# Kernel optimization log

Measured on AMD Instinct MI355X. Metric: run time of the kernel, lower is better.

The kernel has to match this reference:

```python
import jax, jax.numpy as jnp
import numpy as np

EPS = 1e-5
NUM_GROUPS = 32
NUM_HEADS = 4


def setup_inputs() -> dict:
    key = jax.random.key(0)
    ks = jax.random.split(key, 3)
    B, C, H, W = 4, 256, 64, 64
    x = jax.random.normal(ks[0], (B, C, H, W), dtype=jnp.float32)
    gn_w = jnp.ones((C,), jnp.float32)
    gn_b = jnp.zeros((C,), jnp.float32)
    qkv_w = jax.random.normal(ks[1], (3 * C, C), dtype=jnp.float32) * (C ** -0.5)
    qkv_b = jnp.zeros((3 * C,), jnp.float32)
    proj_w = jax.random.normal(ks[2], (C, C), dtype=jnp.float32) * (C ** -0.5)
    proj_b = jnp.zeros((C,), jnp.float32)
    return {"x": x, "gn_w": gn_w, "gn_b": gn_b, "qkv_w": qkv_w,
            "qkv_b": qkv_b, "proj_w": proj_w, "proj_b": proj_b}


def _group_norm(x, w, b):
    B, C, H, W = x.shape
    xg = x.reshape(B, NUM_GROUPS, C // NUM_GROUPS, H, W)
    mean = xg.mean(axis=(2, 3, 4), keepdims=True)
    var = xg.var(axis=(2, 3, 4), keepdims=True)
    xn = ((xg - mean) * jax.lax.rsqrt(var + EPS)).reshape(B, C, H, W)
    return xn * w[None, :, None, None] + b[None, :, None, None]


def reference(x, gn_w, gn_b, qkv_w, qkv_b, proj_w, proj_b):
    B, C, H, W = x.shape
    nh = NUM_HEADS
    d = C // nh
    L = H * W
    h = _group_norm(x, gn_w, gn_b)
    # 1x1 conv == channel matmul
    qkv = jnp.einsum('oc,bchw->bohw', qkv_w, h) + qkv_b[None, :, None, None]
    q, k, v = jnp.split(qkv, 3, axis=1)
    # (B, C, H, W) -> (B, nh, L, d)
    def to_heads(t):
        return t.reshape(B, nh, d, L).transpose(0, 1, 3, 2)
    q, k, v = to_heads(q), to_heads(k), to_heads(v)
    scale = d ** -0.5
    attn = jax.nn.softmax(jnp.einsum('bhqd,bhkd->bhqk', q, k) * scale, axis=-1)
    o = jnp.einsum('bhqk,bhkd->bhqd', attn, v)          # (B, nh, L, d)
    o = o.transpose(0, 1, 3, 2).reshape(B, C, H, W)
    o = jnp.einsum('oc,bchw->bohw', proj_w, o) + proj_b[None, :, None, None]
    return x + o
```

## Files before the change

kernel.cpp:

```cpp
#include <hip/hip_runtime.h>

#define B_   4
#define C_   256
#define L_   4096
#define NH_  4
#define D_   64
#define G_   32
#define CPG_ 8

typedef __bf16 bf16x8 __attribute__((ext_vector_type(8)));
typedef float  f32x4  __attribute__((ext_vector_type(4)));

__device__ __forceinline__ ushort f2bf(float f) {
  union { float f; unsigned u; } c; c.f = f;
  unsigned u = c.u;
  return (ushort)((u + 0x7fffu + ((u >> 16) & 1u)) >> 16);
}
__device__ __forceinline__ float bf2f(ushort h) {
  union { unsigned u; float f; } c; c.u = ((unsigned)h) << 16; return c.f;
}
__device__ __forceinline__ unsigned fbits(float f) {
  union { float f; unsigned u; } c; c.f = f; return c.u;
}
__device__ __forceinline__ float fastexp2(float x) {
#if __has_builtin(__builtin_amdgcn_exp2f)
  return __builtin_amdgcn_exp2f(x);
#else
  return exp2f(x);
#endif
}

__global__ __launch_bounds__(256) void pre_kernel(const float* __restrict__ x,
                                                  const float* __restrict__ wqf,
                                                  const float* __restrict__ wpf,
                                                  ushort* __restrict__ wq,
                                                  ushort* __restrict__ wp,
                                                  float* __restrict__ stats2) {
  int bidx = blockIdx.x;
  int tid  = threadIdx.x;
  if (bidx >= 1024) {
    int t = (bidx - 1024) * 256 + tid;
    const int NQ4 = (768 * 256) / 4;
    float4 v;
    if (t < NQ4) {
      v = ((const float4*)wqf)[t];
      ((ushort4*)wq)[t] = make_ushort4(f2bf(v.x), f2bf(v.y), f2bf(v.z), f2bf(v.w));
    } else {
      int i = t - NQ4;
      v = ((const float4*)wpf)[i];
      ((ushort4*)wp)[i] = make_ushort4(f2bf(v.x), f2bf(v.y), f2bf(v.z), f2bf(v.w));
    }
    return;
  }
  int bg = bidx >> 3, chunk = bidx & 7;
  int b = bg >> 5, g = bg & 31;
  const float* xg = x + ((size_t)b * C_ + g * CPG_) * L_ + chunk * 512;

  float s = 0.f, ss = 0.f;
  for (int c = 0; c < CPG_; ++c) {
    float2 v = ((const float2*)(xg + (size_t)c * L_))[tid];
    s  += v.x + v.y;
    ss += v.x * v.x + v.y * v.y;
  }
  for (int off = 32; off; off >>= 1) { s += __shfl_xor(s, off); ss += __shfl_xor(ss, off); }
  __shared__ float red[8];
  int w = tid >> 6;
  if ((tid & 63) == 0) { red[w] = s; red[4 + w] = ss; }
  __syncthreads();
  if (tid == 0) {
    stats2[bidx * 2]     = red[0] + red[1] + red[2] + red[3];
    stats2[bidx * 2 + 1] = red[4] + red[5] + red[6] + red[7];
  }
}

__global__ __launch_bounds__(256) void qkv_kernel(const float* __restrict__ x,
                                                  const float* __restrict__ stats2,
                                                  const float* __restrict__ gw,
                                                  const float* __restrict__ gb,
                                                  const ushort* __restrict__ w,
                                                  const float* __restrict__ bias,
                                                  ushort* __restrict__ q,
                                                  ushort* __restrict__ k,
                                                  ushort* __restrict__ v) {
  __shared__ __align__(16) ushort h_lds[32][264];

  int tid  = threadIdx.x;
  int wv_  = tid >> 6, lane = tid & 63;
  int quad = lane >> 4, col = lane & 15;
  int bid  = (int)blockIdx.x;
  int b    = bid >> 7;
  int lt   = bid & 127;
  int l0   = lt * 32;

  {
    int ll = tid & 31, chunk = tid >> 5;
    int c0 = chunk * 32;
    const float inv_n = 1.0f / (CPG_ * L_);
    float mean[4], rstd[4];
#pragma unroll
    for (int gg = 0; gg < 4; ++gg) {
      int bg = b * 32 + chunk * 4 + gg;
      float s = 0.f, ss = 0.f;
#pragma unroll
      for (int c2 = 0; c2 < 8; ++c2) {
        s  += stats2[(bg * 8 + c2) * 2];
        ss += stats2[(bg * 8 + c2) * 2 + 1];
      }
      mean[gg] = s * inv_n;
      float var = ss * inv_n - mean[gg] * mean[gg];
      rstd[gg] = rsqrtf(var + 1e-5f);
    }
    int l = l0 + ll;
    union { uint4 u[4]; ushort s[32]; } o;
#pragma unroll
    for (int c = 0; c < 32; ++c) {
      int gg = c >> 3;
      float wvv = gw[c0 + c], bvv = gb[c0 + c];
      float val = x[((size_t)b * C_ + c0 + c) * L_ + l];
      o.s[c] = f2bf((val - mean[gg]) * rstd[gg] * wvv + bvv);
    }
#pragma unroll
    for (int i = 0; i < 4; ++i)
      *(uint4*)&h_lds[ll][c0 + i * 8] = o.u[i];
  }
  __syncthreads();

#pragma unroll
  for (int p = 0; p < 3; ++p) {
    int ot = wv_ + 4 * p;
    int o0 = ot * 64;
    const ushort* abase = w + (size_t)(o0 + col) * C_ + quad * 8;

    f32x4 acc[4][2];
    for (int i = 0; i < 4; ++i) for (int j = 0; j < 2; ++j)
      acc[i][j] = (f32x4){0.f, 0.f, 0.f, 0.f};

#pragma unroll
    for (int k0 = 0; k0 < C_; k0 += 32) {
      bf16x8 a[4], bb[2];
#pragma unroll
      for (int i = 0; i < 4; ++i) a[i]  = *(const bf16x8*)(abase + (size_t)(i * 16) * C_ + k0);
#pragma unroll
      for (int j = 0; j < 2; ++j) bb[j] = *(const bf16x8*)&h_lds[j * 16 + col][k0 + quad * 8];
#pragma unroll
      for (int i = 0; i < 4; ++i)
#pragma unroll
        for (int j = 0; j < 2; ++j)
          acc[i][j] = __builtin_amdgcn_mfma_f32_16x16x32_bf16(a[i], bb[j], acc[i][j], 0, 0, 0);
    }

    int third = o0 >> 8;
    int hh    = (o0 & 255) >> 6;
    float scale = (third == 0) ? 0.180336880111120f : 1.0f;
#pragma unroll
    for (int i = 0; i < 4; ++i) {
      int oo = o0 + i * 16 + quad * 4;
      int dd = i * 16 + quad * 4;
#pragma unroll
      for (int j = 0; j < 2; ++j) {
        int l = l0 + j * 16 + col;
        ushort pk[4];
        for (int r = 0; r < 4; ++r) pk[r] = f2bf((acc[i][j][r] + bias[oo + r]) * scale);
        if (third < 2) {
          ushort* dst = (third ? k : q) + (((size_t)(b * NH_ + hh) * L_ + l) * D_ + dd);
          *(ushort4*)dst = make_ushort4(pk[0], pk[1], pk[2], pk[3]);
        } else {
          for (int r = 0; r < 4; ++r)
            v[((size_t)(b * NH_ + hh) * D_ + dd + r) * L_ + l] = pk[r];
        }
      }
    }
  }
}

__global__ __launch_bounds__(256, 2) void attn_kernel(const ushort* __restrict__ q,
                                                      const ushort* __restrict__ k,
                                                      const ushort* __restrict__ v,
                                                      ushort* __restrict__ p0,
                                                      ushort* __restrict__ p1,
                                                      float* __restrict__ psumbuf) {
  __shared__ __align__(16) ushort k_lds[2][64][72];
  __shared__ __align__(16) ushort v_lds[2][64][72];

  int tid   = threadIdx.x;
  int w     = tid >> 6, lane = tid & 63;
  int quad  = lane >> 4, col = lane & 15;
  int bid   = (int)blockIdx.x;
  bid = (bid & 7) * 64 + (bid >> 3);
  int split = bid >> 8;
  int bh    = (bid >> 4) & 15;
  int qblk  = bid & 15;

  const ushort* qp = q + (size_t)bh * L_ * D_;
  const ushort* kp = k + (size_t)bh * L_ * D_;
  const ushort* vp = v + (size_t)bh * D_ * L_;

  int qrow0 = qblk * 256 + w * 64;
  bf16x8 bq[4][2];
#pragma unroll
  for (int f = 0; f < 4; ++f)
#pragma unroll
    for (int c = 0; c < 2; ++c)
      bq[f][c] = *(const bf16x8*)(qp + (size_t)(qrow0 + f * 16 + col) * D_ + c * 32 + quad * 8);

  f32x4 oacc[4][4];
#pragma unroll
  for (int f = 0; f < 4; ++f)
    for (int t = 0; t < 4; ++t) oacc[f][t] = (f32x4){0.f, 0.f, 0.f, 0.f};
  f32x4 pacc[4];
#pragma unroll
  for (int f = 0; f < 4; ++f) pacc[f] = (f32x4){0.f, 0.f, 0.f, 0.f};
  const f32x4 Z = (f32x4){0.f, 0.f, 0.f, 0.f};

  union { ushort s[8]; bf16x8 v8; } one_u;
#pragma unroll
  for (int i = 0; i < 8; ++i) one_u.s[i] = 0x3F80;
  bf16x8 ones = one_u.v8;

  int vrow = tid >> 2, vchunk = tid & 3;
  int vwoff = (vchunk >> 1) * 32 + (vchunk & 1) * 4;
  int kt0 = split * (L_ / 2), kt_end = kt0 + L_ / 2;

  {
    const uint4* ksrc = (const uint4*)(kp + (size_t)kt0 * D_);
    uint4 a  = ksrc[tid];
    uint4 b2 = ksrc[tid + 256];
    const uint4* vsrc = (const uint4*)(vp + (size_t)vrow * L_ + kt0);
    uint4 c0 = vsrc[vchunk * 2];
    uint4 c1 = vsrc[vchunk * 2 + 1];
    *(uint4*)&k_lds[0][tid >> 3][(tid & 7) * 8] = a;
    *(uint4*)&k_lds[0][32 + (tid >> 3)][(tid & 7) * 8] = b2;
    ushort* vb = &v_lds[0][vrow][vwoff];
    *(uint2*)(vb + 0)  = make_uint2(c0.x, c0.y);
    *(uint2*)(vb + 8)  = make_uint2(c0.z, c0.w);
    *(uint2*)(vb + 16) = make_uint2(c1.x, c1.y);
    *(uint2*)(vb + 24) = make_uint2(c1.z, c1.w);
  }
  __syncthreads();

  int cur = 0;
  for (int kt = kt0; kt < kt_end; kt += 64) {
    bool has_next = (kt + 64) < kt_end;

    f32x4 s[2][4][2];
    __builtin_amdgcn_s_setprio(1);
#pragma unroll
    for (int h = 0; h < 2; ++h) {
      bf16x8 a00 = *(const bf16x8*)&k_lds[cur][h * 32 + col][quad * 8];
      bf16x8 a01 = *(const bf16x8*)&k_lds[cur][h * 32 + col][32 + quad * 8];
      bf16x8 a10 = *(const bf16x8*)&k_lds[cur][h * 32 + 16 + col][quad * 8];
      bf16x8 a11 = *(const bf16x8*)&k_lds[cur][h * 32 + 16 + col][32 + quad * 8];
#pragma unroll
      for (int f = 0; f < 4; ++f) {
        s[h][f][0] = __builtin_amdgcn_mfma_f32_16x16x32_bf16(a00, bq[f][0], Z, 0, 0, 0);
        s[h][f][1] = __builtin_amdgcn_mfma_f32_16x16x32_bf16(a10, bq[f][0], Z, 0, 0, 0);
        s[h][f][0] = __builtin_amdgcn_mfma_f32_16x16x32_bf16(a01, bq[f][1], s[h][f][0], 0, 0, 0);
        s[h][f][1] = __builtin_amdgcn_mfma_f32_16x16x32_bf16(a11, bq[f][1], s[h][f][1], 0, 0, 0);
      }
    }
    __builtin_amdgcn_s_setprio(0);

    uint4 nk0, nk1, nv0, nv1;
    if (has_next) {
      const uint4* ksrc = (const uint4*)(kp + (size_t)(kt + 64) * D_);
      nk0 = ksrc[tid];
      nk1 = ksrc[tid + 256];
      const uint4* vsrc = (const uint4*)(vp + (size_t)vrow * L_ + (kt + 64));
      nv0 = vsrc[vchunk * 2];
      nv1 = vsrc[vchunk * 2 + 1];
    }

#pragma unroll
    for (int h = 0; h < 2; ++h) {
      bf16x8 pb[4];
#pragma unroll
      for (int f = 0; f < 4; ++f) {
        float pe0[4], pe1[4];
#pragma unroll
        for (int r = 0; r < 4; ++r) {
          pe0[r] = fastexp2(s[h][f][0][r]);
          pe1[r] = fastexp2(s[h][f][1][r]);
        }
        union { unsigned u[4]; bf16x8 v8; } pc;
        pc.u[0] = __builtin_amdgcn_perm(fbits(pe0[1]), fbits(pe0[0]), 0x07060302u);
        pc.u[1] = __builtin_amdgcn_perm(fbits(pe0[3]), fbits(pe0[2]), 0x07060302u);
        pc.u[2] = __builtin_amdgcn_perm(fbits(pe1[1]), fbits(pe1[0]), 0x07060302u);
        pc.u[3] = __builtin_amdgcn_perm(fbits(pe1[3]), fbits(pe1[2]), 0x07060302u);
        pb[f] = pc.v8;
      }
#pragma unroll
      for (int f = 0; f < 4; ++f)
        pacc[f] = __builtin_amdgcn_mfma_f32_16x16x32_bf16(ones, pb[f], pacc[f], 0, 0, 0);
#pragma unroll
      for (int t = 0; t < 4; ++t) {
        bf16x8 av = *(const bf16x8*)&v_lds[cur][t * 16 + col][h * 32 + quad * 8];
#pragma unroll
        for (int f = 0; f < 4; ++f)
          oacc[f][t] = __builtin_amdgcn_mfma_f32_16x16x32_bf16(av, pb[f], oacc[f][t], 0, 0, 0);
      }
    }

    if (has_next) {
      int nb = cur ^ 1;
      *(uint4*)&k_lds[nb][tid >> 3][(tid & 7) * 8] = nk0;
      *(uint4*)&k_lds[nb][32 + (tid >> 3)][(tid & 7) * 8] = nk1;
      ushort* vb = &v_lds[nb][vrow][vwoff];
      *(uint2*)(vb + 0)  = make_uint2(nv0.x, nv0.y);
      *(uint2*)(vb + 8)  = make_uint2(nv0.z, nv0.w);
      *(uint2*)(vb + 16) = make_uint2(nv1.x, nv1.y);
      *(uint2*)(vb + 24) = make_uint2(nv1.z, nv1.w);
      __syncthreads();
      cur = nb;
    }
  }

  ushort* po = split ? p1 : p0;
#pragma unroll
  for (int f = 0; f < 4; ++f) {
    for (int t = 0; t < 4; ++t) {
      ushort ok[4];
      for (int r = 0; r < 4; ++r) ok[r] = f2bf(oacc[f][t][r]);
      ushort* dst = po + ((size_t)bh * L_ + qrow0 + f * 16 + col) * D_ + t * 16 + quad * 4;
      *(ushort4*)dst = make_ushort4(ok[0], ok[1], ok[2], ok[3]);
    }
    if (quad == 0)
      psumbuf[split * (16 * L_) + bh * L_ + qrow0 + f * 16 + col] = pacc[f][0];
  }
}

__global__ __launch_bounds__(256) void comb_kernel(ushort* __restrict__ p0,
                                                   const ushort* __restrict__ p1,
                                                   const float* __restrict__ ps) {
  int idx = blockIdx.x * 256 + threadIdx.x;
  int row = idx >> 3;
  float inv = 1.0f / (ps[row] + ps[16 * L_ + row]);
  union { uint4 u; ushort s[8]; } ua, ub, o;
  ua.u = ((const uint4*)p0)[idx];
  ub.u = ((const uint4*)p1)[idx];
#pragma unroll
  for (int e = 0; e < 8; ++e)
    o.s[e] = f2bf((bf2f(ua.s[e]) + bf2f(ub.s[e])) * inv);
  ((uint4*)p0)[idx] = o.u;
}

template<bool FUSED>
__global__ __launch_bounds__(256) void proj_kernel(const ushort* __restrict__ p0,
                                                   const ushort* __restrict__ p1,
                                                   const float* __restrict__ ps,
                                                   const ushort* __restrict__ pw,
                                                   const float* __restrict__ pb,
                                                   const float* __restrict__ x,
                                                   float* __restrict__ out) {
  __shared__ __align__(16) ushort a_lds[32][264];

  int tid  = threadIdx.x;
  int w    = tid >> 6, lane = tid & 63;
  int quad = lane >> 4, col = lane & 15;
  int bid  = (int)blockIdx.x;
  int oct  = (bid & 1) * 4 + w;
  int lt   = (bid >> 1) & 127;
  int b    = bid >> 8;
  int l0 = lt * 32, oc0 = oct * 32;

  if (FUSED) {
    int ll = tid & 31, chunk = tid >> 5;
    int hh = chunk >> 1, d0 = (chunk & 1) * 32;
    size_t row = (size_t)(b * NH_ + hh) * L_ + l0 + ll;
    float inv = 1.0f / (ps[row] + ps[16 * L_ + row]);
    const uint4* s0 = (const uint4*)(p0 + row * D_ + d0);
    const uint4* s1 = (const uint4*)(p1 + row * D_ + d0);
    union { uint4 u[4]; ushort s[32]; } ua, ub, o;
#pragma unroll
    for (int i = 0; i < 4; ++i) { ua.u[i] = s0[i]; ub.u[i] = s1[i]; }
#pragma unroll
    for (int e = 0; e < 32; ++e)
      o.s[e] = f2bf((bf2f(ua.s[e]) + bf2f(ub.s[e])) * inv);
#pragma unroll
    for (int i = 0; i < 4; ++i)
      *(uint4*)&a_lds[ll][chunk * 32 + i * 8] = o.u[i];
    __syncthreads();
  }

  f32x4 acc[2][2];
  for (int i = 0; i < 2; ++i) for (int j = 0; j < 2; ++j)
    acc[i][j] = (f32x4){0.f, 0.f, 0.f, 0.f};

#pragma unroll
  for (int k0 = 0; k0 < C_; k0 += 32) {
    int hh = k0 >> 6, dk = k0 & 63;
    bf16x8 a[2], bb[2];
#pragma unroll
    for (int i = 0; i < 2; ++i) {
      if (FUSED) {
        a[i] = *(const bf16x8*)&a_lds[i * 16 + col][k0 + quad * 8];
      } else {
        a[i] = *(const bf16x8*)(p0 + ((size_t)(b * NH_ + hh) * L_ + l0 + i * 16 + col) * D_ + dk + quad * 8);
      }
    }
#pragma unroll
    for (int j = 0; j < 2; ++j)
      bb[j] = *(const bf16x8*)(pw + (size_t)(oc0 + j * 16 + col) * C_ + k0 + quad * 8);
#pragma unroll
    for (int i = 0; i < 2; ++i)
#pragma unroll
      for (int j = 0; j < 2; ++j)
        acc[i][j] = __builtin_amdgcn_mfma_f32_16x16x32_bf16(a[i], bb[j], acc[i][j], 0, 0, 0);
  }

#pragma unroll
  for (int j = 0; j < 2; ++j) {
    int oc = oc0 + j * 16 + col;
    float bias = pb[oc];
#pragma unroll
    for (int i = 0; i < 2; ++i) {
      int l = l0 + i * 16 + quad * 4;
      size_t off = ((size_t)b * C_ + oc) * L_ + l;
      float4 xv = *(const float4*)(x + off);
      float4 ov = make_float4(acc[i][j][0] + bias + xv.x,
                              acc[i][j][1] + bias + xv.y,
                              acc[i][j][2] + bias + xv.z,
                              acc[i][j][3] + bias + xv.w);
      *(float4*)(out + off) = ov;
    }
  }
}

extern "C" void kernel_launch(void* const* d_in, const int* in_sizes, int n_in,
                              void* d_out, int out_size, void* d_ws, size_t ws_size,
                              hipStream_t stream) {
  const float* x      = (const float*)d_in[0];
  const float* gn_w   = (const float*)d_in[1];
  const float* gn_b   = (const float*)d_in[2];
  const float* qkv_w  = (const float*)d_in[3];
  const float* qkv_b  = (const float*)d_in[4];
  const float* proj_w = (const float*)d_in[5];
  const float* proj_b = (const float*)d_in[6];
  float* out = (float*)d_out;

  const size_t TEN = (size_t)B_ * C_ * L_;
  ushort* ws  = (ushort*)d_ws;
  ushort* q   = ws;
  ushort* k   = ws + TEN;
  ushort* v   = ws + 2 * TEN;
  ushort* oat = ws + 3 * TEN;
  ushort* wq  = ws + 4 * TEN;
  ushort* wp  = wq + 768 * 256;
  ushort* wend = wp + 256 * 256;
  float*  st2 = (float*)((ushort*)d_out + TEN);

  const size_t base_bytes  = (size_t)(wend - ws) * 2;
  const size_t need_fused  = base_bytes + TEN * 2  + (size_t)2 * 16 * L_ * 4 ;
  const bool   fused       = ws_size >= need_fused;

  pre_kernel <<<1280,      256, 0, stream>>>(x, qkv_w, proj_w, wq, wp, st2);
  qkv_kernel <<<512,       256, 0, stream>>>(x, st2, gn_w, gn_b, wq, qkv_b, q, k, v);

  if (fused) {
    ushort* p1w = wend;
    float*  psw = (float*)(wend + TEN);
    attn_kernel<<<512, 256, 0, stream>>>(q, k, v, oat, p1w, psw);
    proj_kernel<true><<<1024, 256, 0, stream>>>(oat, p1w, psw, wp, proj_b, x, out);
  } else {
    ushort* p1d = (ushort*)d_out + TEN;
    float*  psb = (float*)d_out;
    attn_kernel<<<512, 256, 0, stream>>>(q, k, v, oat, p1d, psb);
    comb_kernel<<<2048, 256, 0, stream>>>(oat, p1d, psb);
    proj_kernel<false><<<1024, 256, 0, stream>>>(oat, oat, psb, wp, proj_b, x, out);
  }
}
```

Measured before the change: 191.5 us.

## Merge all stages into one cooperative persistent kernel with grid syncs

Replaces the four separate launches (weight conversion and GroupNorm stats, QKV projection, split-K attention, output projection) with a single cooperative kernel of 512 blocks. Stages are separated by grid.sync(). This removes per-launch overhead and the gaps between kernels. In exchange, every stage now runs at a fixed grid of 512 blocks with two blocks per CU. Each grid barrier also costs time, and the later stages must loop over virtual blocks. If the cooperative launch fails, the code falls back to the old multi-kernel path.

```diff
diff --git a/kernel.cpp b/kernel.cpp
--- a/kernel.cpp
+++ b/kernel.cpp
@@ -1,4 +1,7 @@
 #include <hip/hip_runtime.h>
+#include <hip/hip_cooperative_groups.h>
+
+namespace cg = cooperative_groups;
 
 #define B_   4
 #define C_   256
@@ -28,6 +31,376 @@
 #else
   return exp2f(x);
 #endif
+}
+
+__global__ __launch_bounds__(256, 2) void mega_kernel(
+    const float* __restrict__ x,
+    const float* __restrict__ wqf, const float* __restrict__ wpf,
+    const float* __restrict__ gnw, const float* __restrict__ gnb,
+    const float* __restrict__ qbias, const float* __restrict__ pbias,
+    ushort* wq, ushort* wp, float* st2,
+    ushort* q, ushort* k, ushort* v,
+    ushort* oat, ushort* p1, float* ps,
+    float* out) {
+  __shared__ __align__(16) ushort sm_u[18432];
+
+  cg::grid_group grid = cg::this_grid();
+  int bid0 = (int)blockIdx.x;
+  int tid  = threadIdx.x;
+
+  {
+    float* red = (float*)sm_u;
+    for (int vb = bid0; vb < 1280; vb += 512) {
+      if (vb >= 1024) {
+        int t = (vb - 1024) * 256 + tid;
+        const int NQ4 = (768 * 256) / 4;
+        float4 vv;
+        if (t < NQ4) {
+          vv = ((const float4*)wqf)[t];
+          ((ushort4*)wq)[t] = make_ushort4(f2bf(vv.x), f2bf(vv.y), f2bf(vv.z), f2bf(vv.w));
+        } else {
+          int i = t - NQ4;
+          vv = ((const float4*)wpf)[i];
+          ((ushort4*)wp)[i] = make_ushort4(f2bf(vv.x), f2bf(vv.y), f2bf(vv.z), f2bf(vv.w));
+        }
+        continue;
+      }
+      int bg = vb >> 3, chunk = vb & 7;
+      int b = bg >> 5, g = bg & 31;
+      const float* xg = x + ((size_t)b * C_ + g * CPG_) * L_ + chunk * 512;
+      float s = 0.f, ss = 0.f;
+      for (int c = 0; c < CPG_; ++c) {
+        float2 vv = ((const float2*)(xg + (size_t)c * L_))[tid];
+        s  += vv.x + vv.y;
+        ss += vv.x * vv.x + vv.y * vv.y;
+      }
+      for (int off = 32; off; off >>= 1) { s += __shfl_xor(s, off); ss += __shfl_xor(ss, off); }
+      int w = tid >> 6;
+      if ((tid & 63) == 0) { red[w] = s; red[4 + w] = ss; }
+      __syncthreads();
+      if (tid == 0) {
+        st2[vb * 2]     = red[0] + red[1] + red[2] + red[3];
+        st2[vb * 2 + 1] = red[4] + red[5] + red[6] + red[7];
+      }
+      __syncthreads();
+    }
+  }
+  grid.sync();
+
+  {
+    typedef ushort HRow[264];
+    HRow* h_lds = (HRow*)sm_u;
+
+    int wv_  = tid >> 6, lane = tid & 63;
+    int quad = lane >> 4, col = lane & 15;
+    int b    = bid0 >> 7;
+    int lt   = bid0 & 127;
+    int l0   = lt * 32;
+
+    {
+      int ll = tid & 31, chunk = tid >> 5;
+      int c0 = chunk * 32;
+      const float inv_n = 1.0f / (CPG_ * L_);
+      float mean[4], rstd[4];
+#pragma unroll
+      for (int gg = 0; gg < 4; ++gg) {
+        int bg = b * 32 + chunk * 4 + gg;
+        float s = 0.f, ss = 0.f;
+#pragma unroll
+        for (int c2 = 0; c2 < 8; ++c2) {
+          s  += st2[(bg * 8 + c2) * 2];
+          ss += st2[(bg * 8 + c2) * 2 + 1];
+        }
+        mean[gg] = s * inv_n;
+        float var = ss * inv_n - mean[gg] * mean[gg];
+        rstd[gg] = rsqrtf(var + 1e-5f);
+      }
+      int l = l0 + ll;
+      union { uint4 u[4]; ushort s[32]; } o;
+#pragma unroll
+      for (int c = 0; c < 32; ++c) {
+        int gg = c >> 3;
+        float wvv = gnw[c0 + c], bvv = gnb[c0 + c];
+        float val = x[((size_t)b * C_ + c0 + c) * L_ + l];
+        o.s[c] = f2bf((val - mean[gg]) * rstd[gg] * wvv + bvv);
+      }
+#pragma unroll
+      for (int i = 0; i < 4; ++i)
+        *(uint4*)&h_lds[ll][c0 + i * 8] = o.u[i];
+    }
+    __syncthreads();
+
+#pragma unroll
+    for (int p = 0; p < 3; ++p) {
+      int ot = wv_ + 4 * p;
+      int o0 = ot * 64;
+      const ushort* abase = wq + (size_t)(o0 + col) * C_ + quad * 8;
+
+      f32x4 acc[4][2];
+      for (int i = 0; i < 4; ++i) for (int j = 0; j < 2; ++j)
+        acc[i][j] = (f32x4){0.f, 0.f, 0.f, 0.f};
+
+#pragma unroll
+      for (int k0 = 0; k0 < C_; k0 += 32) {
+        bf16x8 a[4], bb[2];
+#pragma unroll
+        for (int i = 0; i < 4; ++i) a[i]  = *(const bf16x8*)(abase + (size_t)(i * 16) * C_ + k0);
+#pragma unroll
+        for (int j = 0; j < 2; ++j) bb[j] = *(const bf16x8*)&h_lds[j * 16 + col][k0 + quad * 8];
+#pragma unroll
+        for (int i = 0; i < 4; ++i)
+#pragma unroll
+          for (int j = 0; j < 2; ++j)
+            acc[i][j] = __builtin_amdgcn_mfma_f32_16x16x32_bf16(a[i], bb[j], acc[i][j], 0, 0, 0);
+      }
+
+      int third = o0 >> 8;
+      int hh    = (o0 & 255) >> 6;
+      float scale = (third == 0) ? 0.180336880111120f : 1.0f;
+#pragma unroll
+      for (int i = 0; i < 4; ++i) {
+        int oo = o0 + i * 16 + quad * 4;
+        int dd = i * 16 + quad * 4;
+#pragma unroll
+        for (int j = 0; j < 2; ++j) {
+          int l = l0 + j * 16 + col;
+          ushort pk[4];
+          for (int r = 0; r < 4; ++r) pk[r] = f2bf((acc[i][j][r] + qbias[oo + r]) * scale);
+          if (third < 2) {
+            ushort* dst = (third ? k : q) + (((size_t)(b * NH_ + hh) * L_ + l) * D_ + dd);
+            *(ushort4*)dst = make_ushort4(pk[0], pk[1], pk[2], pk[3]);
+          } else {
+            for (int r = 0; r < 4; ++r)
+              v[((size_t)(b * NH_ + hh) * D_ + dd + r) * L_ + l] = pk[r];
+          }
+        }
+      }
+    }
+  }
+  grid.sync();
+
+  {
+    typedef ushort KArr[64][72];
+    KArr* k_lds = (KArr*)sm_u;
+    KArr* v_lds = (KArr*)(sm_u + 2 * 64 * 72);
+
+    int w     = tid >> 6, lane = tid & 63;
+    int quad  = lane >> 4, col = lane & 15;
+    int bid   = (bid0 & 7) * 64 + (bid0 >> 3);
+    int split = bid >> 8;
+    int bh    = (bid >> 4) & 15;
+    int qblk  = bid & 15;
+
+    const ushort* qp = q + (size_t)bh * L_ * D_;
+    const ushort* kp = k + (size_t)bh * L_ * D_;
+    const ushort* vp = v + (size_t)bh * D_ * L_;
+
+    int qrow0 = qblk * 256 + w * 64;
+    bf16x8 bq[4][2];
+#pragma unroll
+    for (int f = 0; f < 4; ++f)
+#pragma unroll
+      for (int c = 0; c < 2; ++c)
+        bq[f][c] = *(const bf16x8*)(qp + (size_t)(qrow0 + f * 16 + col) * D_ + c * 32 + quad * 8);
+
+    f32x4 oacc[4][4];
+#pragma unroll
+    for (int f = 0; f < 4; ++f)
+      for (int t = 0; t < 4; ++t) oacc[f][t] = (f32x4){0.f, 0.f, 0.f, 0.f};
+    f32x4 pacc[4];
+#pragma unroll
+    for (int f = 0; f < 4; ++f) pacc[f] = (f32x4){0.f, 0.f, 0.f, 0.f};
+    const f32x4 Z = (f32x4){0.f, 0.f, 0.f, 0.f};
+
+    union { ushort s[8]; bf16x8 v8; } one_u;
+#pragma unroll
+    for (int i = 0; i < 8; ++i) one_u.s[i] = 0x3F80;
+    bf16x8 ones = one_u.v8;
+
+    int vrow = tid >> 2, vchunk = tid & 3;
+    int vwoff = (vchunk >> 1) * 32 + (vchunk & 1) * 4;
+    int kt0 = split * (L_ / 2), kt_end = kt0 + L_ / 2;
+
+    {
+      const uint4* ksrc = (const uint4*)(kp + (size_t)kt0 * D_);
+      uint4 a  = ksrc[tid];
+      uint4 b2 = ksrc[tid + 256];
+      const uint4* vsrc = (const uint4*)(vp + (size_t)vrow * L_ + kt0);
+      uint4 c0 = vsrc[vchunk * 2];
+      uint4 c1 = vsrc[vchunk * 2 + 1];
+      *(uint4*)&k_lds[0][tid >> 3][(tid & 7) * 8] = a;
+      *(uint4*)&k_lds[0][32 + (tid >> 3)][(tid & 7) * 8] = b2;
+      ushort* vb = &v_lds[0][vrow][vwoff];
+      *(uint2*)(vb + 0)  = make_uint2(c0.x, c0.y);
+      *(uint2*)(vb + 8)  = make_uint2(c0.z, c0.w);
+      *(uint2*)(vb + 16) = make_uint2(c1.x, c1.y);
+      *(uint2*)(vb + 24) = make_uint2(c1.z, c1.w);
+    }
+    __syncthreads();
+
+    int cur = 0;
+    for (int kt = kt0; kt < kt_end; kt += 64) {
+      bool has_next = (kt + 64) < kt_end;
+
+      f32x4 s[2][4][2];
+      __builtin_amdgcn_s_setprio(1);
+#pragma unroll
+      for (int h = 0; h < 2; ++h) {
+        bf16x8 a00 = *(const bf16x8*)&k_lds[cur][h * 32 + col][quad * 8];
+        bf16x8 a01 = *(const bf16x8*)&k_lds[cur][h * 32 + col][32 + quad * 8];
+        bf16x8 a10 = *(const bf16x8*)&k_lds[cur][h * 32 + 16 + col][quad * 8];
+        bf16x8 a11 = *(const bf16x8*)&k_lds[cur][h * 32 + 16 + col][32 + quad * 8];
+#pragma unroll
+        for (int f = 0; f < 4; ++f) {
+          s[h][f][0] = __builtin_amdgcn_mfma_f32_16x16x32_bf16(a00, bq[f][0], Z, 0, 0, 0);
+          s[h][f][1] = __builtin_amdgcn_mfma_f32_16x16x32_bf16(a10, bq[f][0], Z, 0, 0, 0);
+          s[h][f][0] = __builtin_amdgcn_mfma_f32_16x16x32_bf16(a01, bq[f][1], s[h][f][0], 0, 0, 0);
+          s[h][f][1] = __builtin_amdgcn_mfma_f32_16x16x32_bf16(a11, bq[f][1], s[h][f][1], 0, 0, 0);
+        }
+      }
+      __builtin_amdgcn_s_setprio(0);
+
+      uint4 nk0, nk1, nv0, nv1;
+      if (has_next) {
+        const uint4* ksrc = (const uint4*)(kp + (size_t)(kt + 64) * D_);
+        nk0 = ksrc[tid];
+        nk1 = ksrc[tid + 256];
+        const uint4* vsrc = (const uint4*)(vp + (size_t)vrow * L_ + (kt + 64));
+        nv0 = vsrc[vchunk * 2];
+        nv1 = vsrc[vchunk * 2 + 1];
+      }
+
+#pragma unroll
+      for (int h = 0; h < 2; ++h) {
+        bf16x8 pb[4];
+#pragma unroll
+        for (int f = 0; f < 4; ++f) {
+          float pe0[4], pe1[4];
+#pragma unroll
+          for (int r = 0; r < 4; ++r) {
+            pe0[r] = fastexp2(s[h][f][0][r]);
+            pe1[r] = fastexp2(s[h][f][1][r]);
+          }
+          union { unsigned u[4]; bf16x8 v8; } pc;
+          pc.u[0] = __builtin_amdgcn_perm(fbits(pe0[1]), fbits(pe0[0]), 0x07060302u);
+          pc.u[1] = __builtin_amdgcn_perm(fbits(pe0[3]), fbits(pe0[2]), 0x07060302u);
+          pc.u[2] = __builtin_amdgcn_perm(fbits(pe1[1]), fbits(pe1[0]), 0x07060302u);
+          pc.u[3] = __builtin_amdgcn_perm(fbits(pe1[3]), fbits(pe1[2]), 0x07060302u);
+          pb[f] = pc.v8;
+        }
+#pragma unroll
+        for (int f = 0; f < 4; ++f)
+          pacc[f] = __builtin_amdgcn_mfma_f32_16x16x32_bf16(ones, pb[f], pacc[f], 0, 0, 0);
+#pragma unroll
+        for (int t = 0; t < 4; ++t) {
+          bf16x8 av = *(const bf16x8*)&v_lds[cur][t * 16 + col][h * 32 + quad * 8];
+#pragma unroll
+          for (int f = 0; f < 4; ++f)
+            oacc[f][t] = __builtin_amdgcn_mfma_f32_16x16x32_bf16(av, pb[f], oacc[f][t], 0, 0, 0);
+        }
+      }
+
+      if (has_next) {
+        int nb = cur ^ 1;
+        *(uint4*)&k_lds[nb][tid >> 3][(tid & 7) * 8] = nk0;
+        *(uint4*)&k_lds[nb][32 + (tid >> 3)][(tid & 7) * 8] = nk1;
+        ushort* vb = &v_lds[nb][vrow][vwoff];
+        *(uint2*)(vb + 0)  = make_uint2(nv0.x, nv0.y);
+        *(uint2*)(vb + 8)  = make_uint2(nv0.z, nv0.w);
+        *(uint2*)(vb + 16) = make_uint2(nv1.x, nv1.y);
+        *(uint2*)(vb + 24) = make_uint2(nv1.z, nv1.w);
+        __syncthreads();
+        cur = nb;
+      }
+    }
+
+    ushort* po = split ? p1 : oat;
+#pragma unroll
+    for (int f = 0; f < 4; ++f) {
+      for (int t = 0; t < 4; ++t) {
+        ushort ok[4];
+        for (int r = 0; r < 4; ++r) ok[r] = f2bf(oacc[f][t][r]);
+        ushort* dst = po + ((size_t)bh * L_ + qrow0 + f * 16 + col) * D_ + t * 16 + quad * 4;
+        *(ushort4*)dst = make_ushort4(ok[0], ok[1], ok[2], ok[3]);
+      }
+      if (quad == 0)
+        ps[split * (16 * L_) + bh * L_ + qrow0 + f * 16 + col] = pacc[f][0];
+    }
+  }
+  grid.sync();
+
+  {
+    typedef ushort ARow[264];
+    ARow* a_lds = (ARow*)sm_u;
+
+    int w    = tid >> 6, lane = tid & 63;
+    int quad = lane >> 4, col = lane & 15;
+
+    for (int it = 0; it < 2; ++it) {
+      int vb  = bid0 + it * 512;
+      int oct = (vb & 1) * 4 + w;
+      int lt  = (vb >> 1) & 127;
+      int b   = vb >> 8;
+      int l0 = lt * 32, oc0 = oct * 32;
+
+      {
+        int ll = tid & 31, chunk = tid >> 5;
+        int hh = chunk >> 1, d0 = (chunk & 1) * 32;
+        size_t row = (size_t)(b * NH_ + hh) * L_ + l0 + ll;
+        float inv = 1.0f / (ps[row] + ps[16 * L_ + row]);
+        const uint4* s0 = (const uint4*)(oat + row * D_ + d0);
+        const uint4* s1 = (const uint4*)(p1 + row * D_ + d0);
+        union { uint4 u[4]; ushort s[32]; } ua, ub, o;
+#pragma unroll
+        for (int i = 0; i < 4; ++i) { ua.u[i] = s0[i]; ub.u[i] = s1[i]; }
+#pragma unroll
+        for (int e = 0; e < 32; ++e)
+          o.s[e] = f2bf((bf2f(ua.s[e]) + bf2f(ub.s[e])) * inv);
+#pragma unroll
+        for (int i = 0; i < 4; ++i)
+          *(uint4*)&a_lds[ll][chunk * 32 + i * 8] = o.u[i];
+        __syncthreads();
+      }
+
+      f32x4 acc[2][2];
+      for (int i = 0; i < 2; ++i) for (int j = 0; j < 2; ++j)
+        acc[i][j] = (f32x4){0.f, 0.f, 0.f, 0.f};
+
+#pragma unroll
+      for (int k0 = 0; k0 < C_; k0 += 32) {
+        bf16x8 a[2], bb[2];
+#pragma unroll
+        for (int i = 0; i < 2; ++i)
+          a[i] = *(const bf16x8*)&a_lds[i * 16 + col][k0 + quad * 8];
+#pragma unroll
+        for (int j = 0; j < 2; ++j)
+          bb[j] = *(const bf16x8*)(wp + (size_t)(oc0 + j * 16 + col) * C_ + k0 + quad * 8);
+#pragma unroll
+        for (int i = 0; i < 2; ++i)
+#pragma unroll
+          for (int j = 0; j < 2; ++j)
+            acc[i][j] = __builtin_amdgcn_mfma_f32_16x16x32_bf16(a[i], bb[j], acc[i][j], 0, 0, 0);
+      }
+
+#pragma unroll
+      for (int j = 0; j < 2; ++j) {
+        int oc = oc0 + j * 16 + col;
+        float bias = pbias[oc];
+#pragma unroll
+        for (int i = 0; i < 2; ++i) {
+          int l = l0 + i * 16 + quad * 4;
+          size_t off = ((size_t)b * C_ + oc) * L_ + l;
+          float4 xv = *(const float4*)(x + off);
+          float4 ov = make_float4(acc[i][j][0] + bias + xv.x,
+                                  acc[i][j][1] + bias + xv.y,
+                                  acc[i][j][2] + bias + xv.z,
+                                  acc[i][j][3] + bias + xv.w);
+          *(float4*)(out + off) = ov;
+        }
+      }
+      __syncthreads();
+    }
+  }
 }
 
 __global__ __launch_bounds__(256) void pre_kernel(const float* __restrict__ x,
@@ -452,19 +825,38 @@
   const size_t need_fused  = base_bytes + TEN * 2  + (size_t)2 * 16 * L_ * 4 ;
   const bool   fused       = ws_size >= need_fused;
 
-  pre_kernel <<<1280,      256, 0, stream>>>(x, qkv_w, proj_w, wq, wp, st2);
-  qkv_kernel <<<512,       256, 0, stream>>>(x, st2, gn_w, gn_b, wq, qkv_b, q, k, v);
-
+  bool done = false;
   if (fused) {
     ushort* p1w = wend;
     float*  psw = (float*)(wend + TEN);
-    attn_kernel<<<512, 256, 0, stream>>>(q, k, v, oat, p1w, psw);
-    proj_kernel<true><<<1024, 256, 0, stream>>>(oat, p1w, psw, wp, proj_b, x, out);
-  } else {
-    ushort* p1d = (ushort*)d_out + TEN;
-    float*  psb = (float*)d_out;
-    attn_kernel<<<512, 256, 0, stream>>>(q, k, v, oat, p1d, psb);
-    comb_kernel<<<2048, 256, 0, stream>>>(oat, p1d, psb);
-    proj_kernel<false><<<1024, 256, 0, stream>>>(oat, oat, psb, wp, proj_b, x, out);
-  }
-}
+    void* args[] = {
+      (void*)&x, (void*)&qkv_w, (void*)&proj_w,
+      (void*)&gn_w, (void*)&gn_b, (void*)&qkv_b, (void*)&proj_b,
+      (void*)&wq, (void*)&wp, (void*)&st2,
+      (void*)&q, (void*)&k, (void*)&v,
+      (void*)&oat, (void*)&p1w, (void*)&psw,
+      (void*)&out
+    };
+    hipError_t e = hipLaunchCooperativeKernel((const void*)mega_kernel,
+                                              dim3(512), dim3(256),
+                                              args, 0, stream);
+    done = (e == hipSuccess);
+  }
+
+  if (!done) {
+    pre_kernel <<<1280, 256, 0, stream>>>(x, qkv_w, proj_w, wq, wp, st2);
+    qkv_kernel <<<512,  256, 0, stream>>>(x, st2, gn_w, gn_b, wq, qkv_b, q, k, v);
+    if (fused) {
+      ushort* p1w = wend;
+      float*  psw = (float*)(wend + TEN);
+      attn_kernel<<<512, 256, 0, stream>>>(q, k, v, oat, p1w, psw);
+      proj_kernel<true><<<1024, 256, 0, stream>>>(oat, p1w, psw, wp, proj_b, x, out);
+    } else {
+      ushort* p1d = (ushort*)d_out + TEN;
+      float*  psb = (float*)d_out;
+      attn_kernel<<<512, 256, 0, stream>>>(q, k, v, oat, p1d, psb);
+      comb_kernel<<<2048, 256, 0, stream>>>(oat, p1d, psb);
+      proj_kernel<false><<<1024, 256, 0, stream>>>(oat, oat, psb, wp, proj_b, x, out);
+    }
+  }
+}
```

Result: slower. 395.6 us (+106.6%).
